# Performance work log

Hardware: AMD Instinct MI355X
Metric: run time of the kernel (lower is better)

Reference implementation:

```python
import jax, jax.numpy as jnp
import numpy as np

E = 32          # num_experts
D_IN = 1024     # in_features
D_OUT = 1024    # out_features
T = 131072      # total tokens (sum of expert_frequency)


def _make_frequencies():
    # Uneven but deterministic partition of T across E experts (variable group sizes).
    rng = np.random.default_rng(0)
    w = rng.dirichlet(np.ones(E) * 4.0)
    counts = np.floor(w * T).astype(np.int64)
    counts[-1] += T - counts.sum()
    assert counts.sum() == T and (counts >= 0).all()
    return counts


def setup_inputs() -> dict:
    key = jax.random.key(0)
    k_x, k_w = jax.random.split(key)
    x = jax.random.normal(k_x, (T, D_IN), dtype=jnp.float32)
    # nn.init.normal_(weight, mean=0, std=0.02); bias zero-initialized
    weight = jax.random.normal(k_w, (E, D_OUT, D_IN), dtype=jnp.float32) * 0.02
    bias = jnp.zeros((E, D_OUT), dtype=jnp.float32)
    expert_frequency = jnp.asarray(_make_frequencies())
    return {"input": x, "expert_frequency": expert_frequency, "weight": weight, "bias": bias}


def reference(input, expert_frequency, weight, bias):
    # Grouped GEMM: tokens are pre-sorted by expert; group i (of size
    # expert_frequency[i]) is multiplied by weight[i]^T and offset by bias[i].
    # Group sizes are static metadata (torch uses .tolist()), so slicing is static.
    counts = np.asarray(expert_frequency)
    offsets = np.concatenate([[0], np.cumsum(counts)])
    outs = [
        input[offsets[i]:offsets[i + 1]] @ weight[i].T + bias[i]
        for i in range(counts.shape[0])
    ]
    return jnp.concatenate(outs, axis=0)  # [T, D_OUT]
```

## Files before the change

### kernel.cpp

```cpp
#include <hip/hip_runtime.h>
#include <hip/hip_bf16.h>
#include <stdint.h>


#define BM 128
#define BN 128
#define BK 64
#define LDK 72

typedef short v8s __attribute__((ext_vector_type(8)));
typedef float v4f __attribute__((ext_vector_type(4)));

static __device__ __forceinline__ uint32_t pk_bf16(float lo, float hi) {
    union { float f; uint32_t u; } a, b;
    a.f = lo; b.f = hi;
    return __builtin_amdgcn_perm(b.u + 0x8000u, a.u + 0x8000u, 0x07060302u);
}

__global__ __launch_bounds__(256, 2)
void Experts_Cute_54580444398293_kernel(const float* __restrict__ X,
                                        const float* __restrict__ W,
                                        const float* __restrict__ Bias,
                                        const int* __restrict__ counts,
                                        float* __restrict__ Out,
                                        int T, int E, int K, int N) {
    const int nt = blockIdx.x;
    const int mt = blockIdx.y;

    int e = -1, row0 = 0, rows = 0;
    {
        int tacc = 0, off = 0;
        for (int i = 0; i < E; ++i) {
            int c = counts[i];
            int ti = (c + BM - 1) / BM;
            if (mt < tacc + ti) {
                e = i;
                int local = mt - tacc;
                row0 = off + local * BM;
                rows = c - local * BM;
                if (rows > BM) rows = BM;
                break;
            }
            tacc += ti;
            off += c;
        }
    }
    if (e < 0) return;

    __shared__ __align__(16) short As[BM * LDK];
    __shared__ __align__(16) short Bs[BM * LDK];

    const int tid = threadIdx.x;

    const int srow  = tid >> 4;
    const int scol4 = (tid & 15) * 4;

    const int lane = tid & 63;
    const int wv   = tid >> 6;
    const int wm   = (wv >> 1) * 64;
    const int wn   = (wv & 1) * 64;
    const int l16  = lane & 15;
    const int quad = lane >> 4;

    v4f acc[4][4];
#pragma unroll
    for (int i = 0; i < 4; ++i)
#pragma unroll
        for (int j = 0; j < 4; ++j)
            acc[i][j] = (v4f){0.f, 0.f, 0.f, 0.f};

    const float* Wtile = W + ((size_t)e * N + (size_t)nt * BN) * K;
    const int KT = K / BK;

    for (int kt = 0; kt < KT; ++kt) {
        const int k0 = kt * BK;

        {
            v4f ra[8];
            const float* Xp = X + k0 + scol4;
#pragma unroll
            for (int p = 0; p < 8; ++p) {
                int gr = row0 + p * 16 + srow;
                if (gr < T) ra[p] = *(const v4f*)(Xp + (size_t)gr * K);
                else        ra[p] = (v4f){0.f, 0.f, 0.f, 0.f};
            }
#pragma unroll
            for (int p = 0; p < 8; ++p) {
                int r = p * 16 + srow;
                uint32_t w0 = pk_bf16(ra[p].x, ra[p].y);
                uint32_t w1 = pk_bf16(ra[p].z, ra[p].w);
                uint2* dst = (uint2*)&As[r * LDK + scol4];
                *dst = make_uint2(w0, w1);
            }
        }
        {
            v4f rb[8];
            const float* Wp = Wtile + k0 + scol4;
#pragma unroll
            for (int p = 0; p < 8; ++p) {
                int r = p * 16 + srow;
                rb[p] = *(const v4f*)(Wp + (size_t)r * K);
            }
#pragma unroll
            for (int p = 0; p < 8; ++p) {
                int r = p * 16 + srow;
                uint32_t w0 = pk_bf16(rb[p].x, rb[p].y);
                uint32_t w1 = pk_bf16(rb[p].z, rb[p].w);
                uint2* dst = (uint2*)&Bs[r * LDK + scol4];
                *dst = make_uint2(w0, w1);
            }
        }
        __syncthreads();

#pragma unroll
        for (int ks = 0; ks < 2; ++ks) {
            const int koff = ks * 32 + quad * 8;
            v8s af[4], bf[4];
#pragma unroll
            for (int i = 0; i < 4; ++i)
                af[i] = *(const v8s*)&As[(wm + i * 16 + l16) * LDK + koff];
#pragma unroll
            for (int i = 0; i < 4; ++i)
                bf[i] = *(const v8s*)&Bs[(wn + i * 16 + l16) * LDK + koff];
#pragma unroll
            for (int mi = 0; mi < 4; ++mi)
#pragma unroll
                for (int ni = 0; ni < 4; ++ni)
                    acc[mi][ni] = __builtin_amdgcn_mfma_f32_16x16x32_bf16(
                        af[mi], bf[ni], acc[mi][ni], 0, 0, 0);
        }
        if (kt + 1 < KT) __syncthreads();
    }

#pragma unroll
    for (int ni = 0; ni < 4; ++ni) {
        const int col = nt * BN + wn + ni * 16 + l16;
        const float bv = Bias[(size_t)e * N + col];
#pragma unroll
        for (int mi = 0; mi < 4; ++mi) {
            const int rbase = wm + mi * 16 + quad * 4;
#pragma unroll
            for (int rr = 0; rr < 4; ++rr) {
                const int lr = rbase + rr;
                if (lr < rows)
                    Out[(size_t)(row0 + lr) * N + col] = acc[mi][ni][rr] + bv;
            }
        }
    }
}

extern "C" void kernel_launch(void* const* d_in, const int* in_sizes, int n_in,
                              void* d_out, int out_size, void* d_ws, size_t ws_size,
                              hipStream_t stream) {
    const float* X      = (const float*)d_in[0];
    const int*   counts = (const int*)d_in[1];
    const float* W      = (const float*)d_in[2];
    const float* Bias   = (const float*)d_in[3];
    float* Out = (float*)d_out;

    const int E = in_sizes[1];
    const int N = in_sizes[3] / E;
    const int K = in_sizes[2] / in_sizes[3];
    const int T = in_sizes[0] / K;

    const int mtiles = (T + BM - 1) / BM + E;
    dim3 grid(N / BN, mtiles);
    Experts_Cute_54580444398293_kernel<<<grid, 256, 0, stream>>>(
        X, W, Bias, counts, Out, T, E, K, N);
}
```

Measured before the change: 1.453 ms.

## Enlarge tiles to 256x256, double-buffer LDS with register prefetch, swizzle layout

Doubles the block tile to 256x256 with 512 threads, so each wave computes a 128x64 sub-tile and global traffic per FLOP drops. LDS is double-buffered and the next K-slice's global loads are issued before the MFMA loop so they overlap compute. Padded LDS rows are replaced by an XOR swizzle to avoid bank conflicts. Blocks are remapped in chunks of eight for XCD-aware locality, s_setprio is raised around the MFMAs, and output stores are nontemporal. The larger tiles increase register pressure and padding waste on partial expert tiles, and may lower occupancy.

Measured after the change: 1.357 ms. 1.07x faster.

```diff
diff --git a/kernel.cpp b/kernel.cpp
--- a/kernel.cpp
+++ b/kernel.cpp
@@ -1,12 +1,10 @@
 #include <hip/hip_runtime.h>
-#include <hip/hip_bf16.h>
 #include <stdint.h>
 
 
-#define BM 128
-#define BN 128
+#define BM 256
+#define BN 256
 #define BK 64
-#define LDK 72
 
 typedef short v8s __attribute__((ext_vector_type(8)));
 typedef float v4f __attribute__((ext_vector_type(4)));
@@ -17,15 +15,18 @@
     return __builtin_amdgcn_perm(b.u + 0x8000u, a.u + 0x8000u, 0x07060302u);
 }
 
-__global__ __launch_bounds__(256, 2)
+__global__ __launch_bounds__(512, 2)
 void Experts_Cute_54580444398293_kernel(const float* __restrict__ X,
                                         const float* __restrict__ W,
                                         const float* __restrict__ Bias,
                                         const int* __restrict__ counts,
                                         float* __restrict__ Out,
-                                        int T, int E, int K, int N) {
-    const int nt = blockIdx.x;
-    const int mt = blockIdx.y;
+                                        int T, int E, int K, int N, int ntn) {
+    const int nb    = gridDim.x;
+    const int chunk = nb >> 3;
+    const int sw    = (blockIdx.x & 7) * chunk + (blockIdx.x >> 3);
+    const int mt    = sw / ntn;
+    const int nt    = sw - mt * ntn;
 
     int e = -1, row0 = 0, rows = 0;
     {
@@ -47,24 +48,25 @@
     }
     if (e < 0) return;
 
-    __shared__ __align__(16) short As[BM * LDK];
-    __shared__ __align__(16) short Bs[BM * LDK];
+    __shared__ __align__(16) short As[2][BM * BK];
+    __shared__ __align__(16) short Bs[2][BN * BK];
 
     const int tid = threadIdx.x;
 
-    const int srow  = tid >> 4;
-    const int scol4 = (tid & 15) * 4;
+    const int srow = tid >> 4;
+    const int sc16 = tid & 15;
+    const int scol4 = sc16 * 4;
 
     const int lane = tid & 63;
     const int wv   = tid >> 6;
-    const int wm   = (wv >> 1) * 64;
-    const int wn   = (wv & 1) * 64;
+    const int wm   = (wv >> 2) * 128;
+    const int wn   = (wv & 3) * 64;
     const int l16  = lane & 15;
     const int quad = lane >> 4;
 
-    v4f acc[4][4];
+    v4f acc[8][4];
 #pragma unroll
-    for (int i = 0; i < 4; ++i)
+    for (int i = 0; i < 8; ++i)
 #pragma unroll
         for (int j = 0; j < 4; ++j)
             acc[i][j] = (v4f){0.f, 0.f, 0.f, 0.f};
@@ -72,78 +74,95 @@
     const float* Wtile = W + ((size_t)e * N + (size_t)nt * BN) * K;
     const int KT = K / BK;
 
+    v4f ra[8], rb[8];
+
+#define ISSUE_LOADS(k0)                                                     \
+    do {                                                                    \
+        const float* Xp = X + (k0) + scol4;                                 \
+        _Pragma("unroll")                                                   \
+        for (int p = 0; p < 8; ++p) {                                       \
+            int gr = row0 + p * 32 + srow;                                  \
+            if (gr < T) ra[p] = *(const v4f*)(Xp + (size_t)gr * K);         \
+            else        ra[p] = (v4f){0.f, 0.f, 0.f, 0.f};                  \
+        }                                                                   \
+        const float* Wp = Wtile + (k0) + scol4;                             \
+        _Pragma("unroll")                                                   \
+        for (int p = 0; p < 8; ++p)                                         \
+            rb[p] = *(const v4f*)(Wp + (size_t)(p * 32 + srow) * K);        \
+    } while (0)
+
+    ISSUE_LOADS(0);
+    int cur = 0;
+
     for (int kt = 0; kt < KT; ++kt) {
-        const int k0 = kt * BK;
+#pragma unroll
+        for (int p = 0; p < 8; ++p) {
+            int r = p * 32 + srow;
+            uint32_t w0 = pk_bf16(ra[p].x, ra[p].y);
+            uint32_t w1 = pk_bf16(ra[p].z, ra[p].w);
+            int g = (sc16 >> 1) ^ (r & 7);
+            *(uint2*)((char*)As[cur] + r * 128 + g * 16 + (sc16 & 1) * 8) =
+                make_uint2(w0, w1);
+        }
+#pragma unroll
+        for (int p = 0; p < 8; ++p) {
+            int r = p * 32 + srow;
+            uint32_t w0 = pk_bf16(rb[p].x, rb[p].y);
+            uint32_t w1 = pk_bf16(rb[p].z, rb[p].w);
+            int g = (sc16 >> 1) ^ (r & 7);
+            *(uint2*)((char*)Bs[cur] + r * 128 + g * 16 + (sc16 & 1) * 8) =
+                make_uint2(w0, w1);
+        }
 
-        {
-            v4f ra[8];
-            const float* Xp = X + k0 + scol4;
+        if (kt + 1 < KT) ISSUE_LOADS((kt + 1) * BK);
+
+        __syncthreads();
+
+        __builtin_amdgcn_s_setprio(1);
 #pragma unroll
-            for (int p = 0; p < 8; ++p) {
-                int gr = row0 + p * 16 + srow;
-                if (gr < T) ra[p] = *(const v4f*)(Xp + (size_t)gr * K);
-                else        ra[p] = (v4f){0.f, 0.f, 0.f, 0.f};
+        for (int ks = 0; ks < 2; ++ks) {
+            v8s bfr[4];
+#pragma unroll
+            for (int ni = 0; ni < 4; ++ni) {
+                int r = wn + ni * 16 + l16;
+                int g = ((ks * 4 + quad) ^ (r & 7));
+                bfr[ni] = *(const v8s*)((char*)Bs[cur] + r * 128 + g * 16);
             }
 #pragma unroll
-            for (int p = 0; p < 8; ++p) {
-                int r = p * 16 + srow;
-                uint32_t w0 = pk_bf16(ra[p].x, ra[p].y);
-                uint32_t w1 = pk_bf16(ra[p].z, ra[p].w);
-                uint2* dst = (uint2*)&As[r * LDK + scol4];
-                *dst = make_uint2(w0, w1);
+            for (int mh = 0; mh < 2; ++mh) {
+                v8s af[4];
+#pragma unroll
+                for (int i = 0; i < 4; ++i) {
+                    int r = wm + (mh * 4 + i) * 16 + l16;
+                    int g = ((ks * 4 + quad) ^ (r & 7));
+                    af[i] = *(const v8s*)((char*)As[cur] + r * 128 + g * 16);
+                }
+#pragma unroll
+                for (int i = 0; i < 4; ++i)
+#pragma unroll
+                    for (int ni = 0; ni < 4; ++ni)
+                        acc[mh * 4 + i][ni] = __builtin_amdgcn_mfma_f32_16x16x32_bf16(
+                            af[i], bfr[ni], acc[mh * 4 + i][ni], 0, 0, 0);
             }
         }
-        {
-            v4f rb[8];
-            const float* Wp = Wtile + k0 + scol4;
-#pragma unroll
-            for (int p = 0; p < 8; ++p) {
-                int r = p * 16 + srow;
-                rb[p] = *(const v4f*)(Wp + (size_t)r * K);
-            }
-#pragma unroll
-            for (int p = 0; p < 8; ++p) {
-                int r = p * 16 + srow;
-                uint32_t w0 = pk_bf16(rb[p].x, rb[p].y);
-                uint32_t w1 = pk_bf16(rb[p].z, rb[p].w);
-                uint2* dst = (uint2*)&Bs[r * LDK + scol4];
-                *dst = make_uint2(w0, w1);
-            }
-        }
-        __syncthreads();
-
-#pragma unroll
-        for (int ks = 0; ks < 2; ++ks) {
-            const int koff = ks * 32 + quad * 8;
-            v8s af[4], bf[4];
-#pragma unroll
-            for (int i = 0; i < 4; ++i)
-                af[i] = *(const v8s*)&As[(wm + i * 16 + l16) * LDK + koff];
-#pragma unroll
-            for (int i = 0; i < 4; ++i)
-                bf[i] = *(const v8s*)&Bs[(wn + i * 16 + l16) * LDK + koff];
-#pragma unroll
-            for (int mi = 0; mi < 4; ++mi)
-#pragma unroll
-                for (int ni = 0; ni < 4; ++ni)
-                    acc[mi][ni] = __builtin_amdgcn_mfma_f32_16x16x32_bf16(
-                        af[mi], bf[ni], acc[mi][ni], 0, 0, 0);
-        }
-        if (kt + 1 < KT) __syncthreads();
+        __builtin_amdgcn_s_setprio(0);
+        cur ^= 1;
     }
+#undef ISSUE_LOADS
 
 #pragma unroll
     for (int ni = 0; ni < 4; ++ni) {
         const int col = nt * BN + wn + ni * 16 + l16;
         const float bv = Bias[(size_t)e * N + col];
 #pragma unroll
-        for (int mi = 0; mi < 4; ++mi) {
+        for (int mi = 0; mi < 8; ++mi) {
             const int rbase = wm + mi * 16 + quad * 4;
 #pragma unroll
             for (int rr = 0; rr < 4; ++rr) {
                 const int lr = rbase + rr;
                 if (lr < rows)
-                    Out[(size_t)(row0 + lr) * N + col] = acc[mi][ni][rr] + bv;
+                    __builtin_nontemporal_store(acc[mi][ni][rr] + bv,
+                        &Out[(size_t)(row0 + lr) * N + col]);
             }
         }
     }
@@ -163,8 +182,11 @@
     const int K = in_sizes[2] / in_sizes[3];
     const int T = in_sizes[0] / K;
 
-    const int mtiles = (T + BM - 1) / BM + E;
-    dim3 grid(N / BN, mtiles);
-    Experts_Cute_54580444398293_kernel<<<grid, 256, 0, stream>>>(
-        X, W, Bias, counts, Out, T, E, K, N);
+    const int mtmax = (T + BM - 1) / BM + E;
+    const int mt8   = (mtmax + 7) & ~7;
+    const int ntn   = N / BN;
+    const int nb    = ntn * mt8;
+
+    Experts_Cute_54580444398293_kernel<<<dim3(nb), 512, 0, stream>>>(
+        X, W, Bias, counts, Out, T, E, K, N, ntn);
 }
```
